# Optimization experiments

Hardware: AMD Instinct MI355X
Metric: run time of the kernel (lower is better)

The kernel has to match this reference:

```python
import jax, jax.numpy as jnp
import numpy as np

SHIFT_SIZE = 5
PAD = SHIFT_SIZE // 2  # 2
MAX_SHIFT = 2


def conv3x3(x, w, b):
    # x: [B,Cin,H,W], w: [Cout,Cin,3,3]
    y = jax.lax.conv_general_dilated(
        x, w, window_strides=(1, 1), padding='SAME',
        dimension_numbers=('NCHW', 'OIHW', 'NCHW'))
    return y + b[None, :, None, None]


def shift_groups(xn, shifts, axis):
    # xn: [B,C,Hp,Wp]; roll each of the SHIFT_SIZE channel groups by its own shift along `axis`
    B, C, Hp, Wp = xn.shape
    G = shifts.shape[0]
    Cg = C // G
    xg = xn.reshape(B, G, Cg, Hp, Wp)
    rolled = jax.vmap(lambda xc, s: jnp.roll(xc, s, axis=axis),
                      in_axes=(1, 0), out_axes=1)(xg, shifts)  # xc: [B,Cg,Hp,Wp]
    return rolled.reshape(B, C, Hp, Wp)


def setup_inputs() -> dict:
    key = jax.random.key(0)
    ks = jax.random.split(key, 8)
    B, C, H, W = 16, 320, 64, 64
    x = jax.random.normal(ks[0], (B, C, H, W), dtype=jnp.float32)
    edge_guidance = jax.random.normal(ks[1], (B, C, H, W), dtype=jnp.float32)
    w1 = jax.random.normal(ks[2], (16, 1, 3, 3), dtype=jnp.float32) * 0.2
    b1 = jnp.zeros((16,), dtype=jnp.float32)
    w2 = jax.random.normal(ks[3], (2, 16, 3, 3), dtype=jnp.float32) * 0.2
    b2 = jnp.zeros((2,), dtype=jnp.float32)
    shifts_h = jax.random.randint(ks[4], (SHIFT_SIZE,), -MAX_SHIFT, MAX_SHIFT + 1, dtype=jnp.int32)
    shifts_w = jax.random.randint(ks[5], (SHIFT_SIZE,), -MAX_SHIFT, MAX_SHIFT + 1, dtype=jnp.int32)
    return {'x': x, 'edge_guidance': edge_guidance, 'w1': w1, 'b1': b1,
            'w2': w2, 'b2': b2, 'shifts_h': shifts_h, 'shifts_w': shifts_w}


def reference(x, edge_guidance, w1, b1, w2, b2, shifts_h, shifts_w):
    B, C, H, W = x.shape
    # zero-pad spatial dims by PAD on each side
    xn = jnp.pad(x, ((0, 0), (0, 0), (PAD, PAD), (PAD, PAD)))
    # direction gating from edge guidance
    edge_map = jnp.mean(edge_guidance, axis=1, keepdims=True)  # [B,1,H,W]
    h = jax.nn.relu(conv3x3(edge_map, w1, b1))
    dir_logits = conv3x3(h, w2, b2)                            # [B,2,H,W]
    dir_weights = jax.nn.softmax(dir_logits, axis=1)
    # channel-grouped rolls along H and along W, then crop back
    shifted_h = shift_groups(xn, shifts_h, axis=2)[:, :, PAD:PAD + H, PAD:PAD + W]
    shifted_w = shift_groups(xn, shifts_w, axis=3)[:, :, PAD:PAD + H, PAD:PAD + W]
    x_shift = dir_weights[:, 0:1] * shifted_h + dir_weights[:, 1:2] * shifted_w
    return x_shift
```

## Files before the change

### kernel.cpp

```cpp
#include <hip/hip_runtime.h>

#define BATCH 16
#define CHAN  320
#define HH    64
#define WW    64
#define PLANE (HH*WW)
#define NGRP  5
#define CG    64

__device__ float g_em[BATCH * PLANE];
__device__ float g_w0[BATCH * PLANE];

__global__ void k_reduce_mean(const float* __restrict__ eg)
{
    __shared__ float red[256];
    const int bid = blockIdx.x;
    const int b = bid >> 6;
    const int r = bid & 63;
    const int q   = threadIdx.x & 63;
    const int grp = threadIdx.x >> 6;

    const float* p = eg + (((size_t)b * CHAN + (size_t)grp * 80) * PLANE) + r * WW + q;
    float s = 0.f;
#pragma unroll 8
    for (int c = 0; c < 80; ++c)
        s += p[(size_t)c * PLANE];

    red[threadIdx.x] = s;
    __syncthreads();
    if (grp == 0) {
        g_em[(size_t)bid * 64 + q] = red[q] + red[q + 64] + red[q + 128] + red[q + 192];
    }
}

__global__ void k_conv_dir(const float* __restrict__ w1, const float* __restrict__ b1,
                           const float* __restrict__ w2, const float* __restrict__ b2)
{
    __shared__ float sem[20][20];
    __shared__ float shh[18][18];
    __shared__ float sw1[16][9];
    __shared__ float sb1[16];
    __shared__ float sw2[2][16][9];
    __shared__ float sb2[2];

    const int bid = blockIdx.x;
    const int b  = bid >> 4;
    const int t  = bid & 15;
    const int r0 = (t >> 2) * 16;
    const int q0 = (t & 3) * 16;
    const int tid = threadIdx.x;

    if (tid < 144) sw1[tid / 9][tid % 9] = w1[tid];
    if (tid < 16)  sb1[tid] = b1[tid];
    for (int i = tid; i < 288; i += 256) ((float*)sw2)[i] = w2[i];
    if (tid < 2)   sb2[tid] = b2[tid];

    const float scale = 1.0f / (float)CHAN;
    for (int i = tid; i < 400; i += 256) {
        const int lr = i / 20, lq = i % 20;
        const int r = r0 + lr - 2, q = q0 + lq - 2;
        float v = 0.f;
        if ((unsigned)r < HH && (unsigned)q < WW)
            v = g_em[((size_t)b * HH + r) * WW + q] * scale;
        sem[lr][lq] = v;
    }
    __syncthreads();

    const int lr = tid >> 4;
    const int lq = tid & 15;
    float l0 = sb2[0];
    float l1 = sb2[1];

    for (int i = 0; i < 16; ++i) {
        for (int p = tid; p < 324; p += 256) {
            const int hr = p / 18, hq = p % 18;
            const int gr = r0 - 1 + hr, gq = q0 - 1 + hq;
            float acc = 0.f;
            if ((unsigned)gr < HH && (unsigned)gq < WW) {
                acc = sb1[i];
#pragma unroll
                for (int dr = 0; dr < 3; ++dr)
#pragma unroll
                    for (int dq = 0; dq < 3; ++dq)
                        acc += sem[hr + dr][hq + dq] * sw1[i][dr * 3 + dq];
                acc = fmaxf(acc, 0.f);
            }
            shh[hr][hq] = acc;
        }
        __syncthreads();
#pragma unroll
        for (int dr = 0; dr < 3; ++dr)
#pragma unroll
            for (int dq = 0; dq < 3; ++dq) {
                const float hv = shh[lr + dr][lq + dq];
                l0 += hv * sw2[0][i][dr * 3 + dq];
                l1 += hv * sw2[1][i][dr * 3 + dq];
            }
        __syncthreads();
    }

    const float m  = fmaxf(l0, l1);
    const float e0 = expf(l0 - m);
    const float e1 = expf(l1 - m);
    const float w0v = e0 / (e0 + e1);
    g_w0[((size_t)b * HH + (r0 + lr)) * WW + (q0 + lq)] = w0v;
}

__global__ void k_shift_blend(const float* __restrict__ x,
                              const int* __restrict__ sh_arr, const int* __restrict__ sw_arr,
                              float* __restrict__ out)
{
    const int bid = blockIdx.x;
    const int c = bid % CHAN;
    const int b = bid / CHAN;
    const int g = c >> 6;
    const int sh = sh_arr[g];
    const int sw = sw_arr[g];

    const float* xp = x    + (size_t)bid * PLANE;
    const float* wp = g_w0 + (size_t)b * PLANE;
    float*       op = out  + (size_t)bid * PLANE;

#pragma unroll
    for (int j = 0; j < 4; ++j) {
        const int p4 = threadIdx.x + j * 256;
        const int r  = p4 >> 4;
        const int q  = (p4 & 15) * 4;

        const float4 wv = ((const float4*)wp)[p4];

        float4 xh = make_float4(0.f, 0.f, 0.f, 0.f);
        const int rs = r - sh;
        if ((unsigned)rs < HH)
            xh = ((const float4*)(xp + (size_t)rs * WW))[p4 & 15];

        float xw[4];
#pragma unroll
        for (int k = 0; k < 4; ++k) {
            const int qs = q + k - sw;
            xw[k] = ((unsigned)qs < WW) ? xp[r * WW + qs] : 0.f;
        }

        float4 o;
        o.x = wv.x * xh.x + (1.f - wv.x) * xw[0];
        o.y = wv.y * xh.y + (1.f - wv.y) * xw[1];
        o.z = wv.z * xh.z + (1.f - wv.z) * xw[2];
        o.w = wv.w * xh.w + (1.f - wv.w) * xw[3];
        ((float4*)op)[p4] = o;
    }
}

extern "C" void kernel_launch(void* const* d_in, const int* in_sizes, int n_in,
                              void* d_out, int out_size, void* d_ws, size_t ws_size,
                              hipStream_t stream)
{
    const float* x   = (const float*)d_in[0];
    const float* eg  = (const float*)d_in[1];
    const float* w1  = (const float*)d_in[2];
    const float* b1  = (const float*)d_in[3];
    const float* w2  = (const float*)d_in[4];
    const float* b2  = (const float*)d_in[5];
    const int*   shh = (const int*)d_in[6];
    const int*   shw = (const int*)d_in[7];
    float* out = (float*)d_out;

    k_reduce_mean<<<BATCH * HH, 256, 0, stream>>>(eg);
    k_conv_dir<<<BATCH * 16, 256, 0, stream>>>(w1, b1, w2, b2);
    k_shift_blend<<<BATCH * CHAN, 256, 0, stream>>>(x, shh, shw, out);
}
```

Measured before the change: 61.07 us.

## Restructure shift-blend to loop over channels with vectorized shifted loads

The shift-blend kernel now gives each thread a fixed spatial float4 and loops over 16 channels of one group. The direction weight, masks and offsets are computed once per thread and reused across those channels. The W shift is specialized at compile time per shift value, using aligned float4 neighbor loads and lane selection in place of scalar gathers. Outputs use nontemporal stores. The grid shrinks to 1280 blocks, which cuts per-block setup but lowers parallelism.

```diff
diff --git a/kernel.cpp b/kernel.cpp
--- a/kernel.cpp
+++ b/kernel.cpp
@@ -7,6 +7,8 @@
 #define PLANE (HH*WW)
 #define NGRP  5
 #define CG    64
+
+typedef float vfloat4 __attribute__((ext_vector_type(4)));
 
 __device__ float g_em[BATCH * PLANE];
 __device__ float g_w0[BATCH * PLANE];
@@ -106,47 +108,84 @@
     g_w0[((size_t)b * HH + (r0 + lr)) * WW + (q0 + lq)] = w0v;
 }
 
-__global__ void k_shift_blend(const float* __restrict__ x,
-                              const int* __restrict__ sh_arr, const int* __restrict__ sw_arr,
-                              float* __restrict__ out)
-{
+template <int SW>
+__device__ __forceinline__ void sb_loop(const float* pb, float* ob,
+                                        int base, int moff, int hoff,
+                                        float hm, float m0, float m1,
+                                        float m2, float m3, const float4 wv)
+{
+#pragma unroll
+    for (int i = 0; i < 16; ++i) {
+        const float4 xv = *(const float4*)(pb + base);
+        float4 xm = make_float4(0.f, 0.f, 0.f, 0.f);
+        if constexpr (SW != 0)
+            xm = *(const float4*)(pb + moff);
+        const float4 xhl = *(const float4*)(pb + hoff);
+
+        float xw0, xw1, xw2, xw3;
+        if constexpr (SW == 0)      { xw0 = xv.x; xw1 = xv.y; xw2 = xv.z; xw3 = xv.w; }
+        else if constexpr (SW == 1) { xw0 = xm.w; xw1 = xv.x; xw2 = xv.y; xw3 = xv.z; }
+        else if constexpr (SW == 2) { xw0 = xm.z; xw1 = xm.w; xw2 = xv.x; xw3 = xv.y; }
+        else if constexpr (SW == -1){ xw0 = xv.y; xw1 = xv.z; xw2 = xv.w; xw3 = xm.x; }
+        else                        { xw0 = xv.z; xw1 = xv.w; xw2 = xm.x; xw3 = xm.y; }
+        xw0 *= m0; xw1 *= m1; xw2 *= m2; xw3 *= m3;
+
+        vfloat4 o;
+        o.x = xw0 + wv.x * (hm * xhl.x - xw0);
+        o.y = xw1 + wv.y * (hm * xhl.y - xw1);
+        o.z = xw2 + wv.z * (hm * xhl.z - xw2);
+        o.w = xw3 + wv.w * (hm * xhl.w - xw3);
+        __builtin_nontemporal_store(o, (vfloat4*)(ob + base));
+
+        pb += PLANE; ob += PLANE;
+    }
+}
+
+__global__ __launch_bounds__(256) void k_shift_blend(
+        const float* __restrict__ x,
+        const int* __restrict__ sh_arr, const int* __restrict__ sw_arr,
+        float* __restrict__ out)
+{
+    const int tid  = threadIdx.x;
+    const int lane = tid & 63;
+    const int csub = tid >> 6;
+
     const int bid = blockIdx.x;
-    const int c = bid % CHAN;
-    const int b = bid / CHAN;
-    const int g = c >> 6;
-    const int sh = sh_arr[g];
-    const int sw = sw_arr[g];
-
-    const float* xp = x    + (size_t)bid * PLANE;
-    const float* wp = g_w0 + (size_t)b * PLANE;
-    float*       op = out  + (size_t)bid * PLANE;
-
-#pragma unroll
-    for (int j = 0; j < 4; ++j) {
-        const int p4 = threadIdx.x + j * 256;
-        const int r  = p4 >> 4;
-        const int q  = (p4 & 15) * 4;
-
-        const float4 wv = ((const float4*)wp)[p4];
-
-        float4 xh = make_float4(0.f, 0.f, 0.f, 0.f);
-        const int rs = r - sh;
-        if ((unsigned)rs < HH)
-            xh = ((const float4*)(xp + (size_t)rs * WW))[p4 & 15];
-
-        float xw[4];
-#pragma unroll
-        for (int k = 0; k < 4; ++k) {
-            const int qs = q + k - sw;
-            xw[k] = ((unsigned)qs < WW) ? xp[r * WW + qs] : 0.f;
-        }
-
-        float4 o;
-        o.x = wv.x * xh.x + (1.f - wv.x) * xw[0];
-        o.y = wv.y * xh.y + (1.f - wv.y) * xw[1];
-        o.z = wv.z * xh.z + (1.f - wv.z) * xw[2];
-        o.w = wv.w * xh.w + (1.f - wv.w) * xw[3];
-        ((float4*)op)[p4] = o;
+    const int s   = bid & 15;
+    const int g   = (bid >> 4) % NGRP;
+    const int b   = bid / (NGRP * 16);
+    const int sh  = sh_arr[g];
+    const int sw  = sw_arr[g];
+
+    const int p4  = s * 64 + lane;
+    const int r   = p4 >> 4;
+    const int q   = (p4 & 15) * 4;
+    const int base = r * WW + q;
+
+    const int rs  = r - sh;
+    const float hm = ((unsigned)rs < HH) ? 1.f : 0.f;
+    const int rsc = rs < 0 ? 0 : (rs > HH - 1 ? HH - 1 : rs);
+    const int hoff = rsc * WW + q;
+
+    int moff;
+    if (sw > 0) { moff = base - 4; if (moff < 0) moff = 0; }
+    else        { moff = base + 4; if (moff > PLANE - 4) moff = PLANE - 4; }
+
+    float m0 = 1.f, m1 = 1.f, m2 = 1.f, m3 = 1.f;
+    if (q == 0)      { if (sw >= 1) m0 = 0.f; if (sw == 2) m1 = 0.f; }
+    if (q == WW - 4) { if (sw <= -1) m3 = 0.f; if (sw == -2) m2 = 0.f; }
+
+    const int c0 = g * CG + csub * 16;
+    const float* pb = x   + ((size_t)b * CHAN + c0) * PLANE;
+    float*       ob = out + ((size_t)b * CHAN + c0) * PLANE;
+    const float4 wv = *(const float4*)(g_w0 + (size_t)b * PLANE + p4 * 4);
+
+    switch (sw) {
+        case  0: sb_loop< 0>(pb, ob, base, moff, hoff, hm, m0, m1, m2, m3, wv); break;
+        case  1: sb_loop< 1>(pb, ob, base, moff, hoff, hm, m0, m1, m2, m3, wv); break;
+        case  2: sb_loop< 2>(pb, ob, base, moff, hoff, hm, m0, m1, m2, m3, wv); break;
+        case -1: sb_loop<-1>(pb, ob, base, moff, hoff, hm, m0, m1, m2, m3, wv); break;
+        default: sb_loop<-2>(pb, ob, base, moff, hoff, hm, m0, m1, m2, m3, wv); break;
     }
 }
 
@@ -166,5 +205,5 @@
 
     k_reduce_mean<<<BATCH * HH, 256, 0, stream>>>(eg);
     k_conv_dir<<<BATCH * 16, 256, 0, stream>>>(w1, b1, w2, b2);
-    k_shift_blend<<<BATCH * CHAN, 256, 0, stream>>>(x, shh, shw, out);
-}
+    k_shift_blend<<<BATCH * NGRP * 16, 256, 0, stream>>>(x, shh, shw, out);
+}
```

New measurement: 63.55 us. 1.04x slower.

## Restructure shift-blend to reuse per-pixel geometry across channel group with vector loads

Applied to the files above, without the earlier changes.

Each thread now handles one float4 pixel position across 16 channels of its shift group. The row offsets, weight vector and bounds masks are computed once and reused for all 16 channels. The W-shift reads come from two aligned float4 loads (the current and a neighbouring vector) with register selection, replacing four scalar loads. This lowers index arithmetic and scalar memory traffic in the bandwidth-bound blend, at the cost of fewer, longer-running blocks and branchy selects on the shift value.

```diff
diff --git a/kernel.cpp b/kernel.cpp
--- a/kernel.cpp
+++ b/kernel.cpp
@@ -106,47 +106,83 @@
     g_w0[((size_t)b * HH + (r0 + lr)) * WW + (q0 + lq)] = w0v;
 }
 
-__global__ void k_shift_blend(const float* __restrict__ x,
-                              const int* __restrict__ sh_arr, const int* __restrict__ sw_arr,
-                              float* __restrict__ out)
-{
-    const int bid = blockIdx.x;
-    const int c = bid % CHAN;
-    const int b = bid / CHAN;
-    const int g = c >> 6;
-    const int sh = sh_arr[g];
-    const int sw = sw_arr[g];
-
-    const float* xp = x    + (size_t)bid * PLANE;
-    const float* wp = g_w0 + (size_t)b * PLANE;
-    float*       op = out  + (size_t)bid * PLANE;
-
-#pragma unroll
-    for (int j = 0; j < 4; ++j) {
-        const int p4 = threadIdx.x + j * 256;
-        const int r  = p4 >> 4;
-        const int q  = (p4 & 15) * 4;
-
-        const float4 wv = ((const float4*)wp)[p4];
-
-        float4 xh = make_float4(0.f, 0.f, 0.f, 0.f);
-        const int rs = r - sh;
-        if ((unsigned)rs < HH)
-            xh = ((const float4*)(xp + (size_t)rs * WW))[p4 & 15];
-
-        float xw[4];
-#pragma unroll
-        for (int k = 0; k < 4; ++k) {
-            const int qs = q + k - sw;
-            xw[k] = ((unsigned)qs < WW) ? xp[r * WW + qs] : 0.f;
+__device__ __forceinline__ float4 blend4(const float4 v, const float4 m,
+                                         const float4 h, const float4 w,
+                                         const int sw, const int qf,
+                                         const float hm)
+{
+    float xw0 = sw == 2 ? m.z : sw == 1 ? m.w : sw == 0 ? v.x : sw == -1 ? v.y : v.z;
+    float xw1 = sw == 2 ? m.w : sw == 1 ? v.x : sw == 0 ? v.y : sw == -1 ? v.z : v.w;
+    float xw2 = sw == 2 ? v.x : sw == 1 ? v.y : sw == 0 ? v.z : sw == -1 ? v.w : m.x;
+    float xw3 = sw == 2 ? v.y : sw == 1 ? v.z : sw == 0 ? v.w : sw == -1 ? m.x : m.y;
+    xw0 = ((unsigned)(qf + 0 - sw) < WW) ? xw0 : 0.f;
+    xw1 = ((unsigned)(qf + 1 - sw) < WW) ? xw1 : 0.f;
+    xw2 = ((unsigned)(qf + 2 - sw) < WW) ? xw2 : 0.f;
+    xw3 = ((unsigned)(qf + 3 - sw) < WW) ? xw3 : 0.f;
+    float4 o;
+    o.x = xw0 + w.x * (hm * h.x - xw0);
+    o.y = xw1 + w.y * (hm * h.y - xw1);
+    o.z = xw2 + w.z * (hm * h.z - xw2);
+    o.w = xw3 + w.w * (hm * h.w - xw3);
+    return o;
+}
+
+struct K3Geom {
+    int base, moff, hoff, qf, sw;
+    float hm;
+    const float* pb;
+    float* ob;
+    float4 wv;
+};
+
+__device__ __forceinline__ K3Geom k3geom(const float* __restrict__ x,
+                                         float* __restrict__ outp,
+                                         const int* sh_arr, const int* sw_arr)
+{
+    K3Geom gm;
+    const int tid  = threadIdx.x;
+    const int lane = tid & 63;
+    const int csub = tid >> 6;
+    const int bid  = blockIdx.x;
+    const int s    = bid & 15;
+    const int g    = (bid >> 4) % NGRP;
+    const int b    = bid / (NGRP * 16);
+    const int sh   = sh_arr[g];
+    gm.sw          = sw_arr[g];
+
+    const int p4   = s * 64 + lane;
+    const int r    = p4 >> 4;
+    gm.qf          = (p4 & 15) * 4;
+    gm.base        = r * WW + gm.qf;
+    const int rs   = r - sh;
+    gm.hm          = ((unsigned)rs < HH) ? 1.f : 0.f;
+    const int rsc  = rs < 0 ? 0 : (rs > HH - 1 ? HH - 1 : rs);
+    gm.hoff        = rsc * WW + gm.qf;
+    gm.moff        = gm.sw > 0 ? (gm.base - 4 < 0 ? 0 : gm.base - 4)
+                               : (gm.base + 4 > PLANE - 4 ? PLANE - 4 : gm.base + 4);
+    const int c0   = g * CG + csub * 16;
+    gm.pb = x    + ((size_t)b * CHAN + c0) * PLANE;
+    gm.ob = outp + ((size_t)b * CHAN + c0) * PLANE;
+    gm.wv = *(const float4*)(g_w0 + ((size_t)b << 12) + gm.base);
+    return gm;
+}
+
+__global__ __launch_bounds__(256) void k_shift_blend(
+        const float* __restrict__ x, const int* __restrict__ sh_arr,
+        const int* __restrict__ sw_arr, float* __restrict__ out, int npass)
+{
+    K3Geom gm = k3geom(x, out, sh_arr, sw_arr);
+    for (int pass = 0; pass < npass; ++pass) {
+        const float* p = gm.pb; float* o = gm.ob;
+#pragma unroll
+        for (int i = 0; i < 16; ++i) {
+            const float4 a = *(const float4*)(p + gm.base);
+            const float4 m = *(const float4*)(p + gm.moff);
+            const float4 h = *(const float4*)(p + gm.hoff);
+            *(float4*)(o + gm.base) = blend4(a, m, h, gm.wv, gm.sw, gm.qf, gm.hm);
+            p += PLANE; o += PLANE;
         }
-
-        float4 o;
-        o.x = wv.x * xh.x + (1.f - wv.x) * xw[0];
-        o.y = wv.y * xh.y + (1.f - wv.y) * xw[1];
-        o.z = wv.z * xh.z + (1.f - wv.z) * xw[2];
-        o.w = wv.w * xh.w + (1.f - wv.w) * xw[3];
-        ((float4*)op)[p4] = o;
+        asm volatile("" ::: "memory");
     }
 }
 
@@ -166,5 +202,5 @@
 
     k_reduce_mean<<<BATCH * HH, 256, 0, stream>>>(eg);
     k_conv_dir<<<BATCH * 16, 256, 0, stream>>>(w1, b1, w2, b2);
-    k_shift_blend<<<BATCH * CHAN, 256, 0, stream>>>(x, shh, shw, out);
-}
+    k_shift_blend<<<BATCH * NGRP * 16, 256, 0, stream>>>(x, shh, shw, out, 1);
+}
```

Result: slower. 80.80 us (+32.3%).
